# Kernel tuning notes

Measured on AMD Instinct MI355X. Metric: run time of the kernel, lower is better.

Reference implementation:

```python
import jax, jax.numpy as jnp
import numpy as np
from math import sqrt

B, LQ, LKV = 4, 1024, 1024
QD = KD = VD = 1024
MODEL_DIM = 1024
H = 16
HD = MODEL_DIM // H  # per-head model_dim = 64


def setup_inputs() -> dict:
    key = jax.random.key(0)
    ks = jax.random.split(key, 10)
    s = 0.02
    return {
        "queries": jax.random.normal(ks[0], (B, LQ, QD), jnp.float32),
        "context": jax.random.normal(ks[1], (B, LKV, KD), jnp.float32),
        # stacked per-head linear weights (torch Linear: y = x @ W.T + b); store as [H, in, out]
        "Wq": jax.random.normal(ks[2], (H, QD, HD), jnp.float32) * s,
        "bq": jax.random.normal(ks[3], (H, HD), jnp.float32) * s,
        "Wk": jax.random.normal(ks[4], (KD, HD * 1 * H), jnp.float32).reshape(H, KD, HD) * s,
        "bk": jax.random.normal(ks[5], (H, HD), jnp.float32) * s,
        "Wv": jax.random.normal(ks[6], (H, VD, HD), jnp.float32) * s,
        "bv": jax.random.normal(ks[7], (H, HD), jnp.float32) * s,
        "Wo": jax.random.normal(ks[8], (H * HD, MODEL_DIM), jnp.float32) * s,
        "bo": jax.random.normal(ks[9], (MODEL_DIM,), jnp.float32) * s,
    }


def reference(queries, context, Wq, bq, Wk, bk, Wv, bv, Wo, bo):
    # queries: [B,Lq,Dq]; context: [B,Lkv,Dk]
    # Per-head projections, batched over heads (equivalent to the torch per-head loop).
    q = jnp.einsum("bld,hdm->bhlm", queries, Wq) + bq[None, :, None, :]  # [B,H,Lq,hd]
    k = jnp.einsum("bld,hdm->bhlm", context, Wk) + bk[None, :, None, :]  # [B,H,Lkv,hd]
    v = jnp.einsum("bld,hdm->bhlm", context, Wv) + bv[None, :, None, :]  # [B,H,Lkv,hd]

    scale = 1.0 / sqrt(HD)
    scores = jnp.einsum("bhqd,bhkd->bhqk", q, k) * scale  # [B,H,Lq,Lkv]
    att = jax.nn.softmax(scores, axis=-1)
    head_out = jnp.einsum("bhqk,bhkd->bhqd", att, v)  # [B,H,Lq,hd]

    # torch concatenates heads along the last dim in head order 0..H-1
    multi = head_out.transpose(0, 2, 1, 3).reshape(B, LQ, H * HD)
    residual = q.transpose(0, 2, 1, 3).reshape(B, LQ, H * HD)

    out = multi @ Wo + bo  # [B,Lq,model_dim]
    return out, residual
```

## Files before the change

### kernel.cpp

```cpp
#include <hip/hip_runtime.h>
#include <hip/hip_bf16.h>


typedef unsigned short u16;
typedef __attribute__((ext_vector_type(8))) short short8;
typedef __attribute__((ext_vector_type(4))) float f32x4;

__device__ __forceinline__ float bf2f(u16 u) {
    union { unsigned int i; float f; } c;
    c.i = ((unsigned int)u) << 16;
    return c.f;
}

__device__ __forceinline__ u16 f2bf(float f) {
    unsigned int x = __float_as_uint(f);
    unsigned int r = (x + 0x7fffu + ((x >> 16) & 1u)) >> 16;
    return (u16)r;
}

__device__ __forceinline__ void glds16(u16* lds, const u16* g) {
    __builtin_amdgcn_global_load_lds(
        (const __attribute__((address_space(1))) void*)g,
        (__attribute__((address_space(3))) void*)lds, 16, 0, 0);
}

#define FENCE() asm volatile("" ::: "memory")
#define BAR() do { FENCE(); __builtin_amdgcn_s_barrier(); FENCE(); } while (0)
#define WAIT_LGKM0() do { asm volatile("s_waitcnt lgkmcnt(0)" ::: "memory"); \
                          __builtin_amdgcn_sched_barrier(0); } while (0)
#define WAIT_VM4() do { asm volatile("s_waitcnt vmcnt(4)" ::: "memory"); \
                        __builtin_amdgcn_sched_barrier(0); } while (0)
#define WAIT_VM0() do { asm volatile("s_waitcnt vmcnt(0)" ::: "memory"); \
                        __builtin_amdgcn_sched_barrier(0); } while (0)

__global__ __launch_bounds__(256) void prep(
    const float* __restrict__ q, const float* __restrict__ ctx,
    const float* __restrict__ Wq, const float* __restrict__ Wk,
    const float* __restrict__ Wv, const float* __restrict__ Wo,
    u16* __restrict__ Aq, u16* __restrict__ Ac,
    u16* __restrict__ Wqt, u16* __restrict__ Wkt,
    u16* __restrict__ Wvt, u16* __restrict__ Wot)
{
    __shared__ float ls[64][65];
    const int t = threadIdx.x;
    int bid = blockIdx.x;

    if (bid < 4096) {
        const float* in = (bid < 2048) ? q : ctx;
        u16* out = (bid < 2048) ? Aq : Ac;
        size_t i = ((size_t)(bid & 2047) * 256 + t) * 8;
        float4 v0 = *(const float4*)(in + i);
        float4 v1 = *(const float4*)(in + i + 4);
        short8 p;
        p[0] = (short)f2bf(v0.x); p[1] = (short)f2bf(v0.y);
        p[2] = (short)f2bf(v0.z); p[3] = (short)f2bf(v0.w);
        p[4] = (short)f2bf(v1.x); p[5] = (short)f2bf(v1.y);
        p[6] = (short)f2bf(v1.z); p[7] = (short)f2bf(v1.w);
        *(short8*)(out + i) = p;
        return;
    }
    bid -= 4096;
    const float* in; u16* out; int C; size_t moff; int rt, ct;
    if (bid < 768) {
        const int m = bid >> 8, idx = bid & 255;
        in = (m == 0) ? Wq : (m == 1) ? Wk : Wv;
        out = (m == 0) ? Wqt : (m == 1) ? Wkt : Wvt;
        C = 64; rt = (idx & 15) * 64; ct = 0; moff = (size_t)(idx >> 4) * 65536;
    } else {
        const int idx = bid - 768;
        in = Wo; out = Wot; C = 1024; moff = 0;
        rt = (idx & 15) * 64; ct = (idx >> 4) * 64;
    }
    #pragma unroll
    for (int i = 0; i < 4; ++i) {
        int s = i * 256 + t;
        int row = s >> 4, chunk = s & 15;
        float4 v = *(const float4*)(in + moff + (size_t)(rt + row) * C + ct + chunk * 4);
        ls[row][chunk * 4 + 0] = v.x;
        ls[row][chunk * 4 + 1] = v.y;
        ls[row][chunk * 4 + 2] = v.z;
        ls[row][chunk * 4 + 3] = v.w;
    }
    __syncthreads();
    #pragma unroll
    for (int i = 0; i < 2; ++i) {
        int s = i * 256 + t;
        int n = s >> 3, kc = s & 7;
        short8 p;
        #pragma unroll
        for (int j = 0; j < 8; ++j) p[j] = (short)f2bf(ls[kc * 8 + j][n]);
        *(short8*)(out + moff + (size_t)(ct + n) * 1024 + rt + kc * 8) = p;
    }
}

__global__ __launch_bounds__(512) void gemm_qkv8(
    const u16* __restrict__ Aq, const u16* __restrict__ Ac,
    const u16* __restrict__ Wqt, const u16* __restrict__ Wkt,
    const u16* __restrict__ Wvt,
    const float* __restrict__ bq, const float* __restrict__ bk,
    const float* __restrict__ bv,
    u16* __restrict__ qws, u16* __restrict__ kws, u16* __restrict__ vtws)
{
    __shared__ u16 lds[2][2][256 * 64];

    const int tid = threadIdx.x;
    const int w = tid >> 6, lane = tid & 63;
    const int wr = w >> 2, wc = w & 3;
    const int quad = lane >> 4, c = lane & 15, cx = c & 7;
    const int sr = tid >> 3;
    const int gch = (tid & 7) ^ (sr & 7);

    const int f = blockIdx.x;
    const int xcd = f & 7, r = f >> 3;
    const int z = r >> 3;
    const int mt = xcd * 2 + ((r >> 2) & 1);
    const int nt = r & 3;
    const int m0 = mt * 256, n0 = nt * 256;

    const u16* A = (z == 0) ? Aq : Ac;
    const u16* Wt = (z == 0) ? Wqt : (z == 1) ? Wkt : Wvt;
    const float* bias = (z == 0) ? bq : (z == 1) ? bk : bv;

    const u16* gAt = A + (size_t)(m0 + sr) * 1024 + gch * 8;
    const u16* gBt = Wt + (size_t)(n0 + sr) * 1024 + gch * 8;

    auto stageA = [&](int par, int half, int t) {
        const u16* g = gAt + (size_t)half * 128 * 1024 + t * 64;
        u16* l = &lds[par][0][(half * 128 + w * 8) * 64];
        glds16(l, g);
        glds16(l + 64 * 64, g + (size_t)64 * 1024);
    };
    auto stageB = [&](int par, int half, int t) {
        const u16* g = gBt + (size_t)half * 128 * 1024 + t * 64;
        u16* l = &lds[par][1][(half * 128 + w * 8) * 64];
        glds16(l, g);
        glds16(l + 64 * 64, g + (size_t)64 * 1024);
    };

    f32x4 acc[8][4] = {};
    short8 aq[4][2], bA[2][2], bB[2][2];

    auto ldA = [&](int par, int mh) {
        #pragma unroll
        for (int mf = 0; mf < 4; ++mf)
            #pragma unroll
            for (int ks = 0; ks < 2; ++ks)
                aq[mf][ks] = *(const short8*)&lds[par][0][
                    (wr * 128 + mh * 64 + mf * 16 + c) * 64 + (((ks * 4 + quad) ^ cx) * 8)];
    };
    auto ldB = [&](int par, int nh, short8 (&bq_)[2][2]) {
        #pragma unroll
        for (int nf = 0; nf < 2; ++nf)
            #pragma unroll
            for (int ks = 0; ks < 2; ++ks)
                bq_[nf][ks] = *(const short8*)&lds[par][1][
                    (wc * 64 + nh * 32 + nf * 16 + c) * 64 + (((ks * 4 + quad) ^ cx) * 8)];
    };
    auto mma = [&](int mh, int nh, short8 (&bq_)[2][2]) {
        #pragma unroll
        for (int mf = 0; mf < 4; ++mf)
            #pragma unroll
            for (int nf = 0; nf < 2; ++nf)
                #pragma unroll
                for (int ks = 0; ks < 2; ++ks)
                    acc[mh * 4 + mf][nh * 2 + nf] =
                        __builtin_amdgcn_mfma_f32_16x16x32_bf16(
                            aq[mf][ks], bq_[nf][ks], acc[mh * 4 + mf][nh * 2 + nf], 0, 0, 0);
    };

    stageB(0, 0, 0); stageB(0, 1, 0); stageA(0, 0, 0); stageA(0, 1, 0);
    stageB(1, 0, 1); stageB(1, 1, 1);
    WAIT_VM4(); BAR();

    #pragma unroll 1
    for (int i = 0; i < 8; ++i) {
        const int o = 2 * i + 1, e = 2 * i + 2;

        ldA(0, 0); ldB(0, 0, bA);
        stageA(1, 0, o);
        BAR(); WAIT_LGKM0();
        __builtin_amdgcn_s_setprio(1); mma(0, 0, bA); __builtin_amdgcn_s_setprio(0);
        BAR();
        ldB(0, 1, bB);
        stageA(1, 1, o);
        BAR(); WAIT_LGKM0();
        __builtin_amdgcn_s_setprio(1); mma(0, 1, bB); __builtin_amdgcn_s_setprio(0);
        BAR();
        ldA(0, 1);
        if (i < 7) stageB(0, 0, e);
        BAR(); WAIT_LGKM0();
        __builtin_amdgcn_s_setprio(1); mma(1, 1, bB); __builtin_amdgcn_s_setprio(0);
        BAR();
        if (i < 7) stageB(0, 1, e);
        BAR();
        __builtin_amdgcn_s_setprio(1); mma(1, 0, bA); __builtin_amdgcn_s_setprio(0);
        if (i < 7) { WAIT_VM4(); } else { WAIT_VM0(); }
        BAR();
        ldA(1, 0); ldB(1, 0, bA);
        if (i < 7) stageA(0, 0, e);
        BAR(); WAIT_LGKM0();
        __builtin_amdgcn_s_setprio(1); mma(0, 0, bA); __builtin_amdgcn_s_setprio(0);
        BAR();
        ldB(1, 1, bB);
        if (i < 7) stageA(0, 1, e);
        BAR(); WAIT_LGKM0();
        __builtin_amdgcn_s_setprio(1); mma(0, 1, bB); __builtin_amdgcn_s_setprio(0);
        BAR();
        ldA(1, 1);
        if (i < 7) stageB(1, 0, e + 1);
        BAR(); WAIT_LGKM0();
        __builtin_amdgcn_s_setprio(1); mma(1, 1, bB); __builtin_amdgcn_s_setprio(0);
        BAR();
        if (i < 7) stageB(1, 1, e + 1);
        BAR();
        __builtin_amdgcn_s_setprio(1); mma(1, 0, bA); __builtin_amdgcn_s_setprio(0);
        if (i < 7) WAIT_VM4();
        BAR();
    }

    const int h = nt * 4 + wc;
    const int b = m0 >> 10;
    const int lbase = (m0 & 1023) + wr * 128;

    float bb[4];
    #pragma unroll
    for (int cn = 0; cn < 4; ++cn)
        bb[cn] = bias[h * 64 + (cn >> 1) * 32 + (cn & 1) * 16 + c];

    if (z < 2) {
        u16* dst = (z == 0) ? qws : kws;
        const float scale = (z == 0) ? 0.125f : 1.0f;
        u16* dbase = dst + (size_t)(b * 16 + h) * 1024 * 64;
        #pragma unroll
        for (int mi = 0; mi < 8; ++mi) {
            const int ro = (mi >> 2) * 64 + (mi & 3) * 16;
            const int rowb = lbase + ro + quad * 4;
            #pragma unroll
            for (int rr = 0; rr < 4; ++rr) {
                u16* drow = dbase + (size_t)(rowb + rr) * 64;
                #pragma unroll
                for (int cn = 0; cn < 4; ++cn) {
                    const int hd = (cn >> 1) * 32 + (cn & 1) * 16 + c;
                    drow[hd] = f2bf((acc[mi][cn][rr] + bb[cn]) * scale);
                }
            }
        }
    } else {
        u16* dbase = vtws + (size_t)(b * 16 + h) * 64 * 1024;
        #pragma unroll
        for (int mi = 0; mi < 8; ++mi) {
            const int ro = (mi >> 2) * 64 + (mi & 3) * 16;
            const int l0 = lbase + ro + quad * 4;
            #pragma unroll
            for (int cn = 0; cn < 4; ++cn) {
                const int hd = (cn >> 1) * 32 + (cn & 1) * 16 + c;
                ushort4 pk;
                pk.x = f2bf(acc[mi][cn][0] + bb[cn]);
                pk.y = f2bf(acc[mi][cn][1] + bb[cn]);
                pk.z = f2bf(acc[mi][cn][2] + bb[cn]);
                pk.w = f2bf(acc[mi][cn][3] + bb[cn]);
                *(ushort4*)(dbase + (size_t)hd * 1024 + l0) = pk;
            }
        }
    }
}

__global__ __launch_bounds__(256) void gemm_out(
    const u16* __restrict__ A, const u16* __restrict__ Wot,
    const float* __restrict__ bo, float* __restrict__ out)
{
    __shared__ u16 As[128 * 64];
    __shared__ u16 Bs[64 * 64];
    const int f = blockIdx.x;
    const int xcd = f & 7, k = f >> 3;
    const int m0 = (xcd * 4 + (k & 3)) * 128;
    const int n0 = (k >> 2) * 64;
    const int t = threadIdx.x;
    const int w = t >> 6, lane = t & 63;
    const int quad = lane >> 4, c = lane & 15;
    const int cx = c & 7;

    const int sr = w * 8 + (lane >> 3);
    const int gch = (lane & 7) ^ ((lane >> 3) & 7);
    const u16* gA = A + (size_t)(m0 + sr) * 1024 + gch * 8;
    const u16* gB = Wot + (size_t)(n0 + sr) * 1024 + gch * 8;

    const int arow = (w >> 1) * 64 + c;
    const int brow = (w & 1) * 32 + c;

    f32x4 acc[4][2] = {};
    for (int kt = 0; kt < 1024; kt += 64) {
        #pragma unroll
        for (int i = 0; i < 4; ++i)
            glds16(As + (i * 32 + w * 8) * 64, gA + (size_t)i * 32 * 1024 + kt);
        #pragma unroll
        for (int i = 0; i < 2; ++i)
            glds16(Bs + (i * 32 + w * 8) * 64, gB + (size_t)i * 32 * 1024 + kt);
        __syncthreads();
        #pragma unroll
        for (int kh = 0; kh < 2; ++kh) {
            const int ch = (kh * 4 + quad);
            short8 af[4], bf[2];
            #pragma unroll
            for (int rs = 0; rs < 4; ++rs)
                af[rs] = *(const short8*)(As + (arow + rs * 16) * 64 + (ch ^ cx) * 8);
            #pragma unroll
            for (int cs = 0; cs < 2; ++cs)
                bf[cs] = *(const short8*)(Bs + (brow + cs * 16) * 64 + (ch ^ cx) * 8);
            #pragma unroll
            for (int rs = 0; rs < 4; ++rs)
                #pragma unroll
                for (int cs = 0; cs < 2; ++cs)
                    acc[rs][cs] = __builtin_amdgcn_mfma_f32_16x16x32_bf16(
                        af[rs], bf[cs], acc[rs][cs], 0, 0, 0);
        }
        __syncthreads();
    }

    const int nb = n0 + (w & 1) * 32;
    float bb[2];
    #pragma unroll
    for (int cs = 0; cs < 2; ++cs) bb[cs] = bo[nb + cs * 16 + c];

    #pragma unroll
    for (int rs = 0; rs < 4; ++rs) {
        #pragma unroll
        for (int r = 0; r < 4; ++r) {
            const int row = m0 + (w >> 1) * 64 + rs * 16 + quad * 4 + r;
            float* orow = out + (size_t)row * 1024 + nb;
            #pragma unroll
            for (int cs = 0; cs < 2; ++cs)
                orow[cs * 16 + c] = acc[rs][cs][r] + bb[cs];
        }
    }
}

__global__ __launch_bounds__(256) void attn_mfma(
    const u16* __restrict__ qws, const u16* __restrict__ kws,
    const u16* __restrict__ vtws, u16* __restrict__ multi,
    float* __restrict__ resid)
{
    __shared__ u16 Ks[64 * 64];
    __shared__ u16 Vs[64 * 64];
    __shared__ u16 Ps[4][16 * 72];
    const int t = threadIdx.x;
    const int wave = t >> 6, lane = t & 63;
    const int quad = lane >> 4, c = lane & 15;
    const int f = blockIdx.x;
    const int xcd = f & 7, j = f >> 3;
    const int bh = xcd * 8 + (j & 7);
    const int qt = j >> 3;
    const int b = bh >> 4, h = bh & 15;
    const int q0 = qt * 64 + wave * 16;

    const u16* qb = qws + ((size_t)bh * 1024 + q0) * 64;
    const u16* kb = kws + (size_t)bh * 65536;
    const u16* vb = vtws + (size_t)bh * 65536;

    short8 qa0 = *(const short8*)(qb + (size_t)c * 64 + quad * 8);
    short8 qa1 = *(const short8*)(qb + (size_t)c * 64 + 32 + quad * 8);

    const int srow = wave * 16 + (lane >> 3);
    const int gch = (lane & 7) ^ ((lane >> 3) & 7);
    u16* ldsK0 = Ks + (wave * 16) * 64;
    u16* ldsK1 = Ks + (wave * 16 + 8) * 64;
    u16* ldsV0 = Vs + (wave * 16) * 64;
    u16* ldsV1 = Vs + (wave * 16 + 8) * 64;
    const u16* gK0 = kb + (size_t)srow * 64 + gch * 8;
    const u16* gK1 = kb + (size_t)(srow + 8) * 64 + gch * 8;
    const u16* gV0 = vb + (size_t)srow * 1024 + gch * 8;
    const u16* gV1 = vb + (size_t)(srow + 8) * 1024 + gch * 8;

    f32x4 O[4] = {};
    float ps[4] = {0.f, 0.f, 0.f, 0.f};
    u16* pw = &Ps[wave][0];
    const int cx = c & 7;

    for (int kt = 0; kt < 1024; kt += 64) {
        glds16(ldsK0, gK0 + (size_t)kt * 64);
        glds16(ldsK1, gK1 + (size_t)kt * 64);
        glds16(ldsV0, gV0 + kt);
        glds16(ldsV1, gV1 + kt);
        __syncthreads();

        f32x4 s[4];
        #pragma unroll
        for (int nt = 0; nt < 4; ++nt) {
            const u16* kr = Ks + (nt * 16 + c) * 64;
            short8 kb0 = *(const short8*)(kr + ((quad ^ cx)) * 8);
            short8 kb1 = *(const short8*)(kr + (((4 + quad) ^ cx)) * 8);
            f32x4 z = {};
            z = __builtin_amdgcn_mfma_f32_16x16x32_bf16(qa0, kb0, z, 0, 0, 0);
            z = __builtin_amdgcn_mfma_f32_16x16x32_bf16(qa1, kb1, z, 0, 0, 0);
            s[nt] = z;
        }

        #pragma unroll
        for (int nt = 0; nt < 4; ++nt)
            #pragma unroll
            for (int r = 0; r < 4; ++r) {
                float p = __expf(s[nt][r]);
                ps[r] += p;
                pw[(quad * 4 + r) * 72 + nt * 16 + c] = (u16)(__float_as_uint(p) >> 16);
            }
        short8 pa0 = *(const short8*)(pw + c * 72 + quad * 8);
        short8 pa1 = *(const short8*)(pw + c * 72 + 32 + quad * 8);

        #pragma unroll
        for (int nt = 0; nt < 4; ++nt) {
            const u16* vr = Vs + (nt * 16 + c) * 64;
            short8 vb0 = *(const short8*)(vr + ((quad ^ cx)) * 8);
            short8 vb1 = *(const short8*)(vr + (((4 + quad) ^ cx)) * 8);
            O[nt] = __builtin_amdgcn_mfma_f32_16x16x32_bf16(pa0, vb0, O[nt], 0, 0, 0);
            O[nt] = __builtin_amdgcn_mfma_f32_16x16x32_bf16(pa1, vb1, O[nt], 0, 0, 0);
        }
        __syncthreads();
    }

    float inv[4];
    #pragma unroll
    for (int r = 0; r < 4; ++r) {
        float sum = ps[r];
        sum += __shfl_xor(sum, 1);
        sum += __shfl_xor(sum, 2);
        sum += __shfl_xor(sum, 4);
        sum += __shfl_xor(sum, 8);
        inv[r] = 1.0f / sum;
    }

    u16* ob = multi + ((size_t)b * 1024 + q0 + quad * 4) * 1024 + h * 64 + c;
    #pragma unroll
    for (int r = 0; r < 4; ++r) {
        u16* orow = ob + (size_t)r * 1024;
        orow[0]  = f2bf(O[0][r] * inv[r]);
        orow[16] = f2bf(O[1][r] * inv[r]);
        orow[32] = f2bf(O[2][r] * inv[r]);
        orow[48] = f2bf(O[3][r] * inv[r]);
    }

    float* rr = resid + ((size_t)b * 1024 + q0 + c) * 1024 + h * 64;
    #pragma unroll
    for (int jj = 0; jj < 8; ++jj) {
        rr[quad * 8 + jj]      = bf2f((u16)qa0[jj]) * 8.0f;
        rr[32 + quad * 8 + jj] = bf2f((u16)qa1[jj]) * 8.0f;
    }
}

extern "C" void kernel_launch(void* const* d_in, const int* in_sizes, int n_in,
                              void* d_out, int out_size, void* d_ws, size_t ws_size,
                              hipStream_t stream) {
    const float* queries = (const float*)d_in[0];
    const float* context = (const float*)d_in[1];
    const float* Wq = (const float*)d_in[2];
    const float* bq = (const float*)d_in[3];
    const float* Wk = (const float*)d_in[4];
    const float* bk = (const float*)d_in[5];
    const float* Wv = (const float*)d_in[6];
    const float* bv = (const float*)d_in[7];
    const float* Wo = (const float*)d_in[8];
    const float* bo = (const float*)d_in[9];

    float* out = (float*)d_out;
    float* resid = out + (size_t)4 * 1024 * 1024;

    const size_t M1 = 1024 * 1024;
    u16* Aq   = (u16*)d_ws;
    u16* Ac   = Aq + 4 * M1;
    u16* Wqt  = Ac + 4 * M1;
    u16* Wkt  = Wqt + M1;
    u16* Wvt  = Wkt + M1;
    u16* Wot  = Wvt + M1;
    u16* qws  = Wot + M1;
    u16* kws  = qws + 4 * M1;
    u16* vtws = kws + 4 * M1;
    u16* mws  = vtws + 4 * M1;

    prep<<<5120, 256, 0, stream>>>(queries, context, Wq, Wk, Wv, Wo,
                                   Aq, Ac, Wqt, Wkt, Wvt, Wot);
    gemm_qkv8<<<192, 512, 0, stream>>>(Aq, Ac, Wqt, Wkt, Wvt,
                                       bq, bk, bv, qws, kws, vtws);
    attn_mfma<<<1024, 256, 0, stream>>>(qws, kws, vtws, mws, resid);
    gemm_out<<<512, 256, 0, stream>>>(mws, Wot, bo, out);
}
```

Before: 194.2 us.

## Double-buffer LDS tiles in attention and output GEMM with prefetch-ahead loads

Both the output-projection GEMM and the attention kernel now keep two LDS buffers and issue global-to-LDS loads two tiles ahead, waiting with explicit vmcnt counts instead of a full sync after each load. The aim is to hide global memory latency behind the MFMA work. The attention kernel also switches the P scratch buffer from padded rows to an XOR-swizzled layout to avoid bank conflicts, and raises wave priority around the MFMA blocks. LDS use doubles, which may lower occupancy. The hand-set vmcnt thresholds must match the number of outstanding loads exactly.

```diff
diff --git a/kernel.cpp b/kernel.cpp
--- a/kernel.cpp
+++ b/kernel.cpp
@@ -28,6 +28,8 @@
 #define BAR() do { FENCE(); __builtin_amdgcn_s_barrier(); FENCE(); } while (0)
 #define WAIT_LGKM0() do { asm volatile("s_waitcnt lgkmcnt(0)" ::: "memory"); \
                           __builtin_amdgcn_sched_barrier(0); } while (0)
+#define WAIT_VM6() do { asm volatile("s_waitcnt vmcnt(6)" ::: "memory"); \
+                        __builtin_amdgcn_sched_barrier(0); } while (0)
 #define WAIT_VM4() do { asm volatile("s_waitcnt vmcnt(4)" ::: "memory"); \
                         __builtin_amdgcn_sched_barrier(0); } while (0)
 #define WAIT_VM0() do { asm volatile("s_waitcnt vmcnt(0)" ::: "memory"); \
@@ -269,8 +271,8 @@
     const u16* __restrict__ A, const u16* __restrict__ Wot,
     const float* __restrict__ bo, float* __restrict__ out)
 {
-    __shared__ u16 As[128 * 64];
-    __shared__ u16 Bs[64 * 64];
+    __shared__ u16 As[2][128 * 64];
+    __shared__ u16 Bs[2][64 * 64];
     const int f = blockIdx.x;
     const int xcd = f & 7, k = f >> 3;
     const int m0 = (xcd * 4 + (k & 3)) * 128;
@@ -288,25 +290,33 @@
     const int arow = (w >> 1) * 64 + c;
     const int brow = (w & 1) * 32 + c;
 
+    auto stage = [&](int par, int kt) {
+        #pragma unroll
+        for (int i = 0; i < 4; ++i)
+            glds16(As[par] + (i * 32 + w * 8) * 64, gA + (size_t)i * 32 * 1024 + kt);
+        #pragma unroll
+        for (int i = 0; i < 2; ++i)
+            glds16(Bs[par] + (i * 32 + w * 8) * 64, gB + (size_t)i * 32 * 1024 + kt);
+    };
+
     f32x4 acc[4][2] = {};
-    for (int kt = 0; kt < 1024; kt += 64) {
-        #pragma unroll
-        for (int i = 0; i < 4; ++i)
-            glds16(As + (i * 32 + w * 8) * 64, gA + (size_t)i * 32 * 1024 + kt);
-        #pragma unroll
-        for (int i = 0; i < 2; ++i)
-            glds16(Bs + (i * 32 + w * 8) * 64, gB + (size_t)i * 32 * 1024 + kt);
-        __syncthreads();
+    stage(0, 0);
+    stage(1, 64);
+    #pragma unroll 1
+    for (int i = 0; i < 16; ++i) {
+        const int cur = i & 1;
+        if (i < 15) { WAIT_VM6(); } else { WAIT_VM0(); }
+        BAR();
         #pragma unroll
         for (int kh = 0; kh < 2; ++kh) {
             const int ch = (kh * 4 + quad);
             short8 af[4], bf[2];
             #pragma unroll
             for (int rs = 0; rs < 4; ++rs)
-                af[rs] = *(const short8*)(As + (arow + rs * 16) * 64 + (ch ^ cx) * 8);
+                af[rs] = *(const short8*)(As[cur] + (arow + rs * 16) * 64 + (ch ^ cx) * 8);
             #pragma unroll
             for (int cs = 0; cs < 2; ++cs)
-                bf[cs] = *(const short8*)(Bs + (brow + cs * 16) * 64 + (ch ^ cx) * 8);
+                bf[cs] = *(const short8*)(Bs[cur] + (brow + cs * 16) * 64 + (ch ^ cx) * 8);
             #pragma unroll
             for (int rs = 0; rs < 4; ++rs)
                 #pragma unroll
@@ -314,7 +324,8 @@
                     acc[rs][cs] = __builtin_amdgcn_mfma_f32_16x16x32_bf16(
                         af[rs], bf[cs], acc[rs][cs], 0, 0, 0);
         }
-        __syncthreads();
+        BAR();
+        if (i < 14) stage(cur, (i + 2) * 64);
     }
 
     const int nb = n0 + (w & 1) * 32;
@@ -340,12 +351,13 @@
     const u16* __restrict__ vtws, u16* __restrict__ multi,
     float* __restrict__ resid)
 {
-    __shared__ u16 Ks[64 * 64];
-    __shared__ u16 Vs[64 * 64];
-    __shared__ u16 Ps[4][16 * 72];
+    __shared__ u16 Ks[2][64 * 64];
+    __shared__ u16 Vs[2][64 * 64];
+    __shared__ u16 Ps[4][16 * 64];
     const int t = threadIdx.x;
     const int wave = t >> 6, lane = t & 63;
     const int quad = lane >> 4, c = lane & 15;
+    const int cx = c & 7;
     const int f = blockIdx.x;
     const int xcd = f & 7, j = f >> 3;
     const int bh = xcd * 8 + (j & 7);
@@ -362,31 +374,39 @@
 
     const int srow = wave * 16 + (lane >> 3);
     const int gch = (lane & 7) ^ ((lane >> 3) & 7);
-    u16* ldsK0 = Ks + (wave * 16) * 64;
-    u16* ldsK1 = Ks + (wave * 16 + 8) * 64;
-    u16* ldsV0 = Vs + (wave * 16) * 64;
-    u16* ldsV1 = Vs + (wave * 16 + 8) * 64;
     const u16* gK0 = kb + (size_t)srow * 64 + gch * 8;
     const u16* gK1 = kb + (size_t)(srow + 8) * 64 + gch * 8;
     const u16* gV0 = vb + (size_t)srow * 1024 + gch * 8;
     const u16* gV1 = vb + (size_t)(srow + 8) * 1024 + gch * 8;
 
+    auto stage = [&](int par, int kt) {
+        glds16(Ks[par] + (wave * 16) * 64,     gK0 + (size_t)kt * 64);
+        glds16(Ks[par] + (wave * 16 + 8) * 64, gK1 + (size_t)kt * 64);
+        glds16(Vs[par] + (wave * 16) * 64,     gV0 + kt);
+        glds16(Vs[par] + (wave * 16 + 8) * 64, gV1 + kt);
+    };
+
     f32x4 O[4] = {};
     float ps[4] = {0.f, 0.f, 0.f, 0.f};
     u16* pw = &Ps[wave][0];
-    const int cx = c & 7;
-
-    for (int kt = 0; kt < 1024; kt += 64) {
-        glds16(ldsK0, gK0 + (size_t)kt * 64);
-        glds16(ldsK1, gK1 + (size_t)kt * 64);
-        glds16(ldsV0, gV0 + kt);
-        glds16(ldsV1, gV1 + kt);
-        __syncthreads();
+
+    stage(0, 0);
+    stage(1, 64);
+
+    #pragma unroll 1
+    for (int i = 0; i < 16; ++i) {
+        const int cur = i & 1;
+        if (i < 15) { WAIT_VM4(); } else { WAIT_VM0(); }
+        BAR();
+
+        const u16* Kc = Ks[cur];
+        const u16* Vc = Vs[cur];
 
         f32x4 s[4];
+        __builtin_amdgcn_s_setprio(1);
         #pragma unroll
         for (int nt = 0; nt < 4; ++nt) {
-            const u16* kr = Ks + (nt * 16 + c) * 64;
+            const u16* kr = Kc + (nt * 16 + c) * 64;
             short8 kb0 = *(const short8*)(kr + ((quad ^ cx)) * 8);
             short8 kb1 = *(const short8*)(kr + (((4 + quad) ^ cx)) * 8);
             f32x4 z = {};
@@ -394,6 +414,7 @@
             z = __builtin_amdgcn_mfma_f32_16x16x32_bf16(qa1, kb1, z, 0, 0, 0);
             s[nt] = z;
         }
+        __builtin_amdgcn_s_setprio(0);
 
         #pragma unroll
         for (int nt = 0; nt < 4; ++nt)
@@ -401,20 +422,26 @@
             for (int r = 0; r < 4; ++r) {
                 float p = __expf(s[nt][r]);
                 ps[r] += p;
-                pw[(quad * 4 + r) * 72 + nt * 16 + c] = (u16)(__float_as_uint(p) >> 16);
+                const int prow = quad * 4 + r;
+                pw[prow * 64 + (((nt * 2 + (c >> 3)) ^ (prow & 7)) * 8) + (c & 7)]
+                    = (u16)(__float_as_uint(p) >> 16);
             }
-        short8 pa0 = *(const short8*)(pw + c * 72 + quad * 8);
-        short8 pa1 = *(const short8*)(pw + c * 72 + 32 + quad * 8);
-
+        short8 pa0 = *(const short8*)(pw + c * 64 + ((quad ^ cx)) * 8);
+        short8 pa1 = *(const short8*)(pw + c * 64 + (((4 + quad) ^ cx)) * 8);
+
+        __builtin_amdgcn_s_setprio(1);
         #pragma unroll
         for (int nt = 0; nt < 4; ++nt) {
-            const u16* vr = Vs + (nt * 16 + c) * 64;
+            const u16* vr = Vc + (nt * 16 + c) * 64;
             short8 vb0 = *(const short8*)(vr + ((quad ^ cx)) * 8);
             short8 vb1 = *(const short8*)(vr + (((4 + quad) ^ cx)) * 8);
             O[nt] = __builtin_amdgcn_mfma_f32_16x16x32_bf16(pa0, vb0, O[nt], 0, 0, 0);
             O[nt] = __builtin_amdgcn_mfma_f32_16x16x32_bf16(pa1, vb1, O[nt], 0, 0, 0);
         }
-        __syncthreads();
+        __builtin_amdgcn_s_setprio(0);
+
+        BAR();
+        if (i < 14) stage(cur, (i + 2) * 64);
     }
 
     float inv[4];
```

After: 192.1 us. No clear change (-1.1%).
